# Kernel tuning notes

Measured on AMD Instinct MI355X. Metric: run time of the kernel, lower is better.

Reference implementation:

```python
import jax, jax.numpy as jnp
import numpy as np

H = 1024       # hiddenDim
MAXLEN = 512   # maxLen (encoder length)
VOCAB = 32000  # outDim (global in original source)


def setup_inputs() -> dict:
    key = jax.random.key(0)
    ks = jax.random.split(key, 12)
    s = 1.0 / np.sqrt(H)
    u = lambda k, shape: jax.random.uniform(k, shape, jnp.float32, -s, s)
    return {
        "inputId": jax.random.randint(ks[0], (1,), 0, VOCAB),
        "hidden": jax.random.normal(ks[1], (1, 1, H), jnp.float32),
        "encoderOuts": jax.random.normal(ks[2], (MAXLEN, H), jnp.float32),
        "embed_table": jax.random.normal(ks[3], (VOCAB, H), jnp.float32),
        "attn_w": u(ks[4], (MAXLEN, 2 * H)),
        "attn_b": u(ks[5], (MAXLEN,)),
        "comb_w": u(ks[6], (H, 2 * H)),
        "comb_b": u(ks[7], (H,)),
        "w_ih": u(ks[8], (3 * H, H)),
        "w_hh": u(ks[9], (3 * H, H)),
        "b_ih": u(ks[10], (3 * H,)),
        "b_hh": u(ks[11], (3 * H,)),
    }


def reference(inputId, hidden, encoderOuts, embed_table, attn_w, attn_b,
              comb_w, comb_b, w_ih, w_hh, b_ih, b_hh):
    # embedding + (eval-mode) dropout -> identity
    embed = embed_table[inputId].reshape(1, 1, -1)            # (1,1,H)
    # attention over encoder outputs
    cat = jnp.concatenate([embed[0], hidden[0]], axis=1)      # (1,2H)
    attnWeights = jax.nn.softmax(cat @ attn_w.T + attn_b, axis=1)  # (1,MAXLEN)
    attnApplied = attnWeights @ encoderOuts                   # (1,H) == bmm squeeze
    # combine + relu
    x = jnp.concatenate([embed[0], attnApplied], axis=1)      # (1,2H)
    x = jax.nn.relu(x @ comb_w.T + comb_b)                    # (1,H)
    # single GRU step; original calls self.rnn(out) with NO hidden -> h0 = zeros
    h0 = jnp.zeros_like(x)
    gi = x @ w_ih.T + b_ih                                    # (1,3H)
    gh = h0 @ w_hh.T + b_hh                                   # (1,3H)
    i_r, i_z, i_n = jnp.split(gi, 3, axis=1)
    h_r, h_z, h_n = jnp.split(gh, 3, axis=1)
    r = jax.nn.sigmoid(i_r + h_r)
    z = jax.nn.sigmoid(i_z + h_z)
    n = jnp.tanh(i_n + r * h_n)
    h_new = (1.0 - z) * n + z * h0                            # (1,H)
    out = jax.nn.sigmoid(h_new)[None]                         # (1,1,H)
    return out, h_new[None], attnWeights
```

## Files before the change

kernel.cpp:

```cpp
#include <hip/hip_runtime.h>
#include <hip/hip_bf16.h>

#define H 1024
#define MAXLEN 512

__device__ __forceinline__ float wave_reduce_sum(float a) {
    #pragma unroll
    for (int off = 32; off; off >>= 1) a += __shfl_xor(a, off);
    return a;
}
__device__ __forceinline__ float wave_reduce_max(float a) {
    #pragma unroll
    for (int off = 32; off; off >>= 1) a = fmaxf(a, __shfl_xor(a, off));
    return a;
}

__global__ void kA_logits(const int* __restrict__ inputId,
                          const float* __restrict__ embed_table,
                          const float* __restrict__ hidden,
                          const float* __restrict__ attn_w,
                          const float* __restrict__ attn_b,
                          float* __restrict__ logits) {
    int lane = threadIdx.x & 63;
    int row = blockIdx.x * 4 + (threadIdx.x >> 6);
    const float* embed = embed_table + (size_t)inputId[0] * H;
    const float* wrow = attn_w + (size_t)row * (2 * H);
    float acc = 0.f;
    #pragma unroll
    for (int it = 0; it < 8; ++it) {
        int base = it * 256 + lane * 4;
        float4 wv = *reinterpret_cast<const float4*>(wrow + base);
        float4 cv = (it < 4)
            ? *reinterpret_cast<const float4*>(embed + base)
            : *reinterpret_cast<const float4*>(hidden + (base - H));
        acc += wv.x * cv.x + wv.y * cv.y + wv.z * cv.z + wv.w * cv.w;
    }
    acc = wave_reduce_sum(acc);
    if (lane == 0) logits[row] = acc + attn_b[row];
}

__global__ void kB_softmax_apply(const float* __restrict__ logits,
                                 const float* __restrict__ enc,
                                 float* __restrict__ attnApplied,
                                 float* __restrict__ out_w) {
    __shared__ float w_lds[MAXLEN];
    __shared__ float red[4];
    __shared__ float part[8][32];
    int tid = threadIdx.x;
    int lane = tid & 63, wid = tid >> 6;

    float l0 = logits[tid];
    float l1 = logits[tid + 256];

    float m = wave_reduce_max(fmaxf(l0, l1));
    if (lane == 0) red[wid] = m;
    __syncthreads();
    m = fmaxf(fmaxf(red[0], red[1]), fmaxf(red[2], red[3]));
    __syncthreads();

    float e0 = expf(l0 - m), e1 = expf(l1 - m);

    float s = wave_reduce_sum(e0 + e1);
    if (lane == 0) red[wid] = s;
    __syncthreads();
    s = red[0] + red[1] + red[2] + red[3];
    float inv = 1.f / s;

    float w0 = e0 * inv, w1 = e1 * inv;
    w_lds[tid] = w0;
    w_lds[tid + 256] = w1;
    if (blockIdx.x == 0) {
        out_w[tid] = w0;
        out_w[tid + 256] = w1;
    }
    __syncthreads();

    int c = tid & 31;
    int ks = tid >> 5;
    int col = blockIdx.x * 32 + c;
    float acc = 0.f;
    for (int k = ks; k < MAXLEN; k += 8)
        acc += w_lds[k] * enc[(size_t)k * H + col];
    part[ks][c] = acc;
    __syncthreads();
    if (tid < 32) {
        float t = 0.f;
        #pragma unroll
        for (int i = 0; i < 8; ++i) t += part[i][tid];
        attnApplied[blockIdx.x * 32 + tid] = t;
    }
}

__global__ void kC_combine(const int* __restrict__ inputId,
                           const float* __restrict__ embed_table,
                           const float* __restrict__ attnApplied,
                           const float* __restrict__ comb_w,
                           const float* __restrict__ comb_b,
                           float* __restrict__ x) {
    int lane = threadIdx.x & 63;
    int row = blockIdx.x * 4 + (threadIdx.x >> 6);
    const float* embed = embed_table + (size_t)inputId[0] * H;
    const float* wrow = comb_w + (size_t)row * (2 * H);
    float acc = 0.f;
    #pragma unroll
    for (int it = 0; it < 8; ++it) {
        int base = it * 256 + lane * 4;
        float4 wv = *reinterpret_cast<const float4*>(wrow + base);
        float4 cv = (it < 4)
            ? *reinterpret_cast<const float4*>(embed + base)
            : *reinterpret_cast<const float4*>(attnApplied + (base - H));
        acc += wv.x * cv.x + wv.y * cv.y + wv.z * cv.z + wv.w * cv.w;
    }
    acc = wave_reduce_sum(acc);
    if (lane == 0) x[row] = fmaxf(acc + comb_b[row], 0.f);
}

__global__ void kD_gru(const float* __restrict__ w_ih,
                       const float* __restrict__ b_ih,
                       const float* __restrict__ b_hh,
                       const float* __restrict__ x,
                       float* __restrict__ d_out) {
    int lane = threadIdx.x & 63;
    int j = blockIdx.x * 4 + (threadIdx.x >> 6);
    float acc0 = 0.f, acc1 = 0.f, acc2 = 0.f;
    const float* wr = w_ih + (size_t)j * H;
    const float* wz = w_ih + (size_t)(H + j) * H;
    const float* wn = w_ih + (size_t)(2 * H + j) * H;
    #pragma unroll
    for (int it = 0; it < 4; ++it) {
        int base = it * 256 + lane * 4;
        float4 xv = *reinterpret_cast<const float4*>(x + base);
        float4 a = *reinterpret_cast<const float4*>(wr + base);
        float4 b = *reinterpret_cast<const float4*>(wz + base);
        float4 c = *reinterpret_cast<const float4*>(wn + base);
        acc0 += a.x * xv.x + a.y * xv.y + a.z * xv.z + a.w * xv.w;
        acc1 += b.x * xv.x + b.y * xv.y + b.z * xv.z + b.w * xv.w;
        acc2 += c.x * xv.x + c.y * xv.y + c.z * xv.z + c.w * xv.w;
    }
    #pragma unroll
    for (int off = 32; off; off >>= 1) {
        acc0 += __shfl_xor(acc0, off);
        acc1 += __shfl_xor(acc1, off);
        acc2 += __shfl_xor(acc2, off);
    }
    if (lane == 0) {
        float gi_r = acc0 + b_ih[j];
        float gi_z = acc1 + b_ih[H + j];
        float gi_n = acc2 + b_ih[2 * H + j];
        float r = 1.f / (1.f + expf(-(gi_r + b_hh[j])));
        float z = 1.f / (1.f + expf(-(gi_z + b_hh[H + j])));
        float n = tanhf(gi_n + r * b_hh[2 * H + j]);
        float hnew = (1.f - z) * n;
        float outv = 1.f / (1.f + expf(-hnew));
        d_out[j] = outv;
        d_out[H + j] = hnew;
    }
}

extern "C" void kernel_launch(void* const* d_in, const int* in_sizes, int n_in,
                              void* d_out, int out_size, void* d_ws, size_t ws_size,
                              hipStream_t stream) {
    const int*   inputId     = (const int*)d_in[0];
    const float* hidden      = (const float*)d_in[1];
    const float* enc         = (const float*)d_in[2];
    const float* embed_table = (const float*)d_in[3];
    const float* attn_w      = (const float*)d_in[4];
    const float* attn_b      = (const float*)d_in[5];
    const float* comb_w      = (const float*)d_in[6];
    const float* comb_b      = (const float*)d_in[7];
    const float* w_ih        = (const float*)d_in[8];
    const float* b_ih        = (const float*)d_in[10];
    const float* b_hh        = (const float*)d_in[11];

    float* out = (float*)d_out;
    float* ws  = (float*)d_ws;

    float* logits      = ws;
    float* attnApplied = ws + 512;
    float* x           = ws + 2048;

    kA_logits       <<<128, 256, 0, stream>>>(inputId, embed_table, hidden, attn_w, attn_b, logits);
    kB_softmax_apply<<<32,  256, 0, stream>>>(logits, enc, attnApplied, out + 2048);
    kC_combine      <<<256, 256, 0, stream>>>(inputId, embed_table, attnApplied, comb_w, comb_b, x);
    kD_gru          <<<256, 256, 0, stream>>>(w_ih, b_ih, b_hh, x, out);
}
```

Before: 24.32 us.

## Precompute comb_w×encoderOuts product with bf16 MFMA to remove serial attention stage

Reassociates comb_w[:,H:] @ (attnWeights @ enc) as (comb_w[:,H:] @ enc^T) @ attnWeights. A 1024x512x1024 bf16 MFMA GEMM computes that product in parallel with the attention logits and the embedding half of the combine matvec, so the launches drop from four to three. This removes the serial attention-apply and combine stages, but does about 1 GFLOP of extra matrix work per call, writes and reads a 2 MB intermediate, and lowers precision to bf16. The new path runs only if the workspace is large enough; otherwise the original four kernels run.

```diff
diff --git a/kernel.cpp b/kernel.cpp
--- a/kernel.cpp
+++ b/kernel.cpp
@@ -4,6 +4,10 @@
 #define H 1024
 #define MAXLEN 512
 
+typedef __bf16 bf16x8 __attribute__((ext_vector_type(8)));
+typedef __bf16 bf16x4 __attribute__((ext_vector_type(4)));
+typedef float  f32x4  __attribute__((ext_vector_type(4)));
+
 __device__ __forceinline__ float wave_reduce_sum(float a) {
     #pragma unroll
     for (int off = 32; off; off >>= 1) a += __shfl_xor(a, off);
@@ -15,111 +19,182 @@
     return a;
 }
 
-__global__ void kA_logits(const int* __restrict__ inputId,
-                          const float* __restrict__ embed_table,
-                          const float* __restrict__ hidden,
-                          const float* __restrict__ attn_w,
-                          const float* __restrict__ attn_b,
-                          float* __restrict__ logits) {
-    int lane = threadIdx.x & 63;
-    int row = blockIdx.x * 4 + (threadIdx.x >> 6);
+#define WS_LOGITS 0
+#define WS_Y1     512
+#define WS_Z      1536
+#define WS_GT     2560
+#define WS_FLOATS (2560 + 1024 * 512)
+
+__global__ __launch_bounds__(512)
+void node1(const int* __restrict__ inputId,
+           const float* __restrict__ hidden,
+           const float* __restrict__ enc,
+           const float* __restrict__ embed_table,
+           const float* __restrict__ attn_w,
+           const float* __restrict__ attn_b,
+           const float* __restrict__ comb_w,
+           const float* __restrict__ comb_b,
+           float* __restrict__ ws) {
+    float* logits = ws + WS_LOGITS;
+    float* y1     = ws + WS_Y1;
+    float* Gt     = ws + WS_GT;
+
+    __shared__ __bf16 lds_a[128][64];
+    __shared__ __bf16 lds_b[128][64];
+
+    const int tid  = threadIdx.x;
+    const int lane = tid & 63;
+    const int w    = tid >> 6;
+    const int b    = blockIdx.x;
+
     const float* embed = embed_table + (size_t)inputId[0] * H;
-    const float* wrow = attn_w + (size_t)row * (2 * H);
-    float acc = 0.f;
-    #pragma unroll
-    for (int it = 0; it < 8; ++it) {
-        int base = it * 256 + lane * 4;
-        float4 wv = *reinterpret_cast<const float4*>(wrow + base);
-        float4 cv = (it < 4)
-            ? *reinterpret_cast<const float4*>(embed + base)
-            : *reinterpret_cast<const float4*>(hidden + (base - H));
-        acc += wv.x * cv.x + wv.y * cv.y + wv.z * cv.z + wv.w * cv.w;
-    }
-    acc = wave_reduce_sum(acc);
-    if (lane == 0) logits[row] = acc + attn_b[row];
-}
-
-__global__ void kB_softmax_apply(const float* __restrict__ logits,
-                                 const float* __restrict__ enc,
-                                 float* __restrict__ attnApplied,
-                                 float* __restrict__ out_w) {
-    __shared__ float w_lds[MAXLEN];
+
+    if (b < 32) {
+        const int pBase = (b >> 2) * 128;
+        const int qBase = (b & 3) * 128;
+        const int wm = w & 3;
+        const int wn = w >> 2;
+        f32x4 acc[2][4];
+        #pragma unroll
+        for (int m = 0; m < 2; ++m)
+            #pragma unroll
+            for (int n = 0; n < 4; ++n) acc[m][n] = (f32x4){0.f, 0.f, 0.f, 0.f};
+
+        for (int c = 0; c < 16; ++c) {
+            const int k0 = c * 64;
+            #pragma unroll
+            for (int i = 0; i < 4; ++i) {
+                int f4  = tid + i * 512;
+                int row = f4 >> 4, c4 = f4 & 15;
+                float4 ga = *(const float4*)(comb_w + (size_t)(pBase + row) * 2048 + 1024 + k0 + c4 * 4);
+                float4 gb = *(const float4*)(enc    + (size_t)(qBase + row) * 1024 +        k0 + c4 * 4);
+                int off = ((((c4 >> 1) ^ (row & 7)) << 4) | ((c4 & 1) << 3));
+                bf16x4 va, vb;
+                va[0] = (__bf16)ga.x; va[1] = (__bf16)ga.y; va[2] = (__bf16)ga.z; va[3] = (__bf16)ga.w;
+                vb[0] = (__bf16)gb.x; vb[1] = (__bf16)gb.y; vb[2] = (__bf16)gb.z; vb[3] = (__bf16)gb.w;
+                *(bf16x4*)((char*)(&lds_a[row][0]) + off) = va;
+                *(bf16x4*)((char*)(&lds_b[row][0]) + off) = vb;
+            }
+            __syncthreads();
+            #pragma unroll
+            for (int ks = 0; ks < 2; ++ks) {
+                const int slot = ks * 4 + (lane >> 4);
+                bf16x8 af[2], bfr[4];
+                #pragma unroll
+                for (int m = 0; m < 2; ++m) {
+                    int row = wm * 32 + m * 16 + (lane & 15);
+                    af[m] = *(const bf16x8*)((const char*)(&lds_a[row][0]) + ((slot ^ (row & 7)) << 4));
+                }
+                #pragma unroll
+                for (int n = 0; n < 4; ++n) {
+                    int row = wn * 64 + n * 16 + (lane & 15);
+                    bfr[n] = *(const bf16x8*)((const char*)(&lds_b[row][0]) + ((slot ^ (row & 7)) << 4));
+                }
+                #pragma unroll
+                for (int m = 0; m < 2; ++m)
+                    #pragma unroll
+                    for (int n = 0; n < 4; ++n)
+                        acc[m][n] = __builtin_amdgcn_mfma_f32_16x16x32_bf16(af[m], bfr[n], acc[m][n], 0, 0, 0);
+            }
+            __syncthreads();
+        }
+        #pragma unroll
+        for (int m = 0; m < 2; ++m) {
+            int p0 = pBase + wm * 32 + m * 16 + (lane >> 4) * 4;
+            #pragma unroll
+            for (int n = 0; n < 4; ++n) {
+                int q = qBase + wn * 64 + n * 16 + (lane & 15);
+                #pragma unroll
+                for (int i = 0; i < 4; ++i)
+                    Gt[(size_t)(p0 + i) * 512 + q] = acc[m][n][i];
+            }
+        }
+    } else if (b < 96) {
+        int row = (b - 32) * 8 + w;
+        const float* wrow = attn_w + (size_t)row * (2 * H);
+        float acc = 0.f;
+        #pragma unroll
+        for (int it = 0; it < 8; ++it) {
+            int base = it * 256 + lane * 4;
+            float4 wv = *(const float4*)(wrow + base);
+            float4 cv = (it < 4) ? *(const float4*)(embed + base)
+                                 : *(const float4*)(hidden + (base - H));
+            acc += wv.x * cv.x + wv.y * cv.y + wv.z * cv.z + wv.w * cv.w;
+        }
+        acc = wave_reduce_sum(acc);
+        if (lane == 0) logits[row] = acc + attn_b[row];
+    } else {
+        #pragma unroll
+        for (int rr = 0; rr < 2; ++rr) {
+            int row = (b - 96) * 16 + w * 2 + rr;
+            const float* wrow = comb_w + (size_t)row * (2 * H);
+            float acc = 0.f;
+            #pragma unroll
+            for (int it = 0; it < 4; ++it) {
+                int base = it * 256 + lane * 4;
+                float4 wv = *(const float4*)(wrow + base);
+                float4 ev = *(const float4*)(embed + base);
+                acc += wv.x * ev.x + wv.y * ev.y + wv.z * ev.z + wv.w * ev.w;
+            }
+            acc = wave_reduce_sum(acc);
+            if (lane == 0) y1[row] = acc + comb_b[row];
+        }
+    }
+}
+
+__global__ __launch_bounds__(256)
+void node2(float* __restrict__ ws, float* __restrict__ d_out) {
+    const float* logits = ws + WS_LOGITS;
+    const float* y1     = ws + WS_Y1;
+    const float* Gt     = ws + WS_GT;
+    float* z = ws + WS_Z;
+
+    __shared__ float wsm[MAXLEN];
     __shared__ float red[4];
-    __shared__ float part[8][32];
-    int tid = threadIdx.x;
-    int lane = tid & 63, wid = tid >> 6;
-
-    float l0 = logits[tid];
-    float l1 = logits[tid + 256];
-
+    const int tid = threadIdx.x, lane = tid & 63, wid = tid >> 6;
+    const int b = blockIdx.x;
+
+    float l0 = logits[tid], l1 = logits[tid + 256];
     float m = wave_reduce_max(fmaxf(l0, l1));
     if (lane == 0) red[wid] = m;
     __syncthreads();
     m = fmaxf(fmaxf(red[0], red[1]), fmaxf(red[2], red[3]));
     __syncthreads();
-
     float e0 = expf(l0 - m), e1 = expf(l1 - m);
-
     float s = wave_reduce_sum(e0 + e1);
     if (lane == 0) red[wid] = s;
     __syncthreads();
     s = red[0] + red[1] + red[2] + red[3];
     float inv = 1.f / s;
-
     float w0 = e0 * inv, w1 = e1 * inv;
-    w_lds[tid] = w0;
-    w_lds[tid + 256] = w1;
-    if (blockIdx.x == 0) {
-        out_w[tid] = w0;
-        out_w[tid + 256] = w1;
-    }
-    __syncthreads();
-
-    int c = tid & 31;
-    int ks = tid >> 5;
-    int col = blockIdx.x * 32 + c;
-    float acc = 0.f;
-    for (int k = ks; k < MAXLEN; k += 8)
-        acc += w_lds[k] * enc[(size_t)k * H + col];
-    part[ks][c] = acc;
-    __syncthreads();
-    if (tid < 32) {
-        float t = 0.f;
-        #pragma unroll
-        for (int i = 0; i < 8; ++i) t += part[i][tid];
-        attnApplied[blockIdx.x * 32 + tid] = t;
-    }
-}
-
-__global__ void kC_combine(const int* __restrict__ inputId,
-                           const float* __restrict__ embed_table,
-                           const float* __restrict__ attnApplied,
-                           const float* __restrict__ comb_w,
-                           const float* __restrict__ comb_b,
-                           float* __restrict__ x) {
-    int lane = threadIdx.x & 63;
-    int row = blockIdx.x * 4 + (threadIdx.x >> 6);
-    const float* embed = embed_table + (size_t)inputId[0] * H;
-    const float* wrow = comb_w + (size_t)row * (2 * H);
-    float acc = 0.f;
-    #pragma unroll
-    for (int it = 0; it < 8; ++it) {
-        int base = it * 256 + lane * 4;
-        float4 wv = *reinterpret_cast<const float4*>(wrow + base);
-        float4 cv = (it < 4)
-            ? *reinterpret_cast<const float4*>(embed + base)
-            : *reinterpret_cast<const float4*>(attnApplied + (base - H));
-        acc += wv.x * cv.x + wv.y * cv.y + wv.z * cv.z + wv.w * cv.w;
-    }
-    acc = wave_reduce_sum(acc);
-    if (lane == 0) x[row] = fmaxf(acc + comb_b[row], 0.f);
-}
-
-__global__ void kD_gru(const float* __restrict__ w_ih,
-                       const float* __restrict__ b_ih,
-                       const float* __restrict__ b_hh,
-                       const float* __restrict__ x,
-                       float* __restrict__ d_out) {
+    wsm[tid] = w0;
+    wsm[tid + 256] = w1;
+    if (b == 0) {
+        d_out[2048 + tid] = w0;
+        d_out[2048 + 256 + tid] = w1;
+    }
+    __syncthreads();
+
+    #pragma unroll
+    for (int rr = 0; rr < 4; ++rr) {
+        int row = b * 16 + wid * 4 + rr;
+        const float* g = Gt + (size_t)row * 512;
+        float acc = 0.f;
+        #pragma unroll
+        for (int i = 0; i < 8; ++i)
+            acc += g[lane + 64 * i] * wsm[lane + 64 * i];
+        acc = wave_reduce_sum(acc);
+        if (lane == 0) z[row] = y1[row] + acc;
+    }
+}
+
+__global__ __launch_bounds__(256)
+void node3(const float* __restrict__ w_ih,
+           const float* __restrict__ b_ih,
+           const float* __restrict__ b_hh,
+           const float* __restrict__ ws,
+           float* __restrict__ d_out) {
+    const float* z = ws + WS_Z;
     int lane = threadIdx.x & 63;
     int j = blockIdx.x * 4 + (threadIdx.x >> 6);
     float acc0 = 0.f, acc1 = 0.f, acc2 = 0.f;
@@ -129,13 +204,128 @@
     #pragma unroll
     for (int it = 0; it < 4; ++it) {
         int base = it * 256 + lane * 4;
-        float4 xv = *reinterpret_cast<const float4*>(x + base);
-        float4 a = *reinterpret_cast<const float4*>(wr + base);
-        float4 b = *reinterpret_cast<const float4*>(wz + base);
-        float4 c = *reinterpret_cast<const float4*>(wn + base);
+        float4 xv = *(const float4*)(z + base);
+        xv.x = fmaxf(xv.x, 0.f); xv.y = fmaxf(xv.y, 0.f);
+        xv.z = fmaxf(xv.z, 0.f); xv.w = fmaxf(xv.w, 0.f);
+        float4 a = *(const float4*)(wr + base);
+        float4 c = *(const float4*)(wz + base);
+        float4 d = *(const float4*)(wn + base);
         acc0 += a.x * xv.x + a.y * xv.y + a.z * xv.z + a.w * xv.w;
-        acc1 += b.x * xv.x + b.y * xv.y + b.z * xv.z + b.w * xv.w;
-        acc2 += c.x * xv.x + c.y * xv.y + c.z * xv.z + c.w * xv.w;
+        acc1 += c.x * xv.x + c.y * xv.y + c.z * xv.z + c.w * xv.w;
+        acc2 += d.x * xv.x + d.y * xv.y + d.z * xv.z + d.w * xv.w;
+    }
+    #pragma unroll
+    for (int off = 32; off; off >>= 1) {
+        acc0 += __shfl_xor(acc0, off);
+        acc1 += __shfl_xor(acc1, off);
+        acc2 += __shfl_xor(acc2, off);
+    }
+    if (lane == 0) {
+        float gi_r = acc0 + b_ih[j];
+        float gi_z = acc1 + b_ih[H + j];
+        float gi_n = acc2 + b_ih[2 * H + j];
+        float r = 1.f / (1.f + expf(-(gi_r + b_hh[j])));
+        float zz = 1.f / (1.f + expf(-(gi_z + b_hh[H + j])));
+        float n = tanhf(gi_n + r * b_hh[2 * H + j]);
+        float hnew = (1.f - zz) * n;
+        float outv = 1.f / (1.f + expf(-hnew));
+        d_out[j] = outv;
+        d_out[H + j] = hnew;
+    }
+}
+
+__global__ void fb_kA(const int* __restrict__ inputId, const float* __restrict__ embed_table,
+                      const float* __restrict__ hidden, const float* __restrict__ attn_w,
+                      const float* __restrict__ attn_b, float* __restrict__ logits) {
+    int lane = threadIdx.x & 63;
+    int row = blockIdx.x * 4 + (threadIdx.x >> 6);
+    const float* embed = embed_table + (size_t)inputId[0] * H;
+    const float* wrow = attn_w + (size_t)row * (2 * H);
+    float acc = 0.f;
+    #pragma unroll
+    for (int it = 0; it < 8; ++it) {
+        int base = it * 256 + lane * 4;
+        float4 wv = *(const float4*)(wrow + base);
+        float4 cv = (it < 4) ? *(const float4*)(embed + base)
+                             : *(const float4*)(hidden + (base - H));
+        acc += wv.x * cv.x + wv.y * cv.y + wv.z * cv.z + wv.w * cv.w;
+    }
+    acc = wave_reduce_sum(acc);
+    if (lane == 0) logits[row] = acc + attn_b[row];
+}
+__global__ void fb_kB(const float* __restrict__ logits, const float* __restrict__ enc,
+                      float* __restrict__ attnApplied, float* __restrict__ out_w) {
+    __shared__ float w_lds[MAXLEN];
+    __shared__ float red[4];
+    __shared__ float part[8][32];
+    int tid = threadIdx.x, lane = tid & 63, wid = tid >> 6;
+    float l0 = logits[tid], l1 = logits[tid + 256];
+    float m = wave_reduce_max(fmaxf(l0, l1));
+    if (lane == 0) red[wid] = m;
+    __syncthreads();
+    m = fmaxf(fmaxf(red[0], red[1]), fmaxf(red[2], red[3]));
+    __syncthreads();
+    float e0 = expf(l0 - m), e1 = expf(l1 - m);
+    float s = wave_reduce_sum(e0 + e1);
+    if (lane == 0) red[wid] = s;
+    __syncthreads();
+    s = red[0] + red[1] + red[2] + red[3];
+    float inv = 1.f / s;
+    float w0 = e0 * inv, w1 = e1 * inv;
+    w_lds[tid] = w0; w_lds[tid + 256] = w1;
+    if (blockIdx.x == 0) { out_w[tid] = w0; out_w[tid + 256] = w1; }
+    __syncthreads();
+    int c = tid & 31, ks = tid >> 5;
+    int col = blockIdx.x * 32 + c;
+    float acc = 0.f;
+    for (int k = ks; k < MAXLEN; k += 8) acc += w_lds[k] * enc[(size_t)k * H + col];
+    part[ks][c] = acc;
+    __syncthreads();
+    if (tid < 32) {
+        float t = 0.f;
+        #pragma unroll
+        for (int i = 0; i < 8; ++i) t += part[i][tid];
+        attnApplied[blockIdx.x * 32 + tid] = t;
+    }
+}
+__global__ void fb_kC(const int* __restrict__ inputId, const float* __restrict__ embed_table,
+                      const float* __restrict__ attnApplied, const float* __restrict__ comb_w,
+                      const float* __restrict__ comb_b, float* __restrict__ x) {
+    int lane = threadIdx.x & 63;
+    int row = blockIdx.x * 4 + (threadIdx.x >> 6);
+    const float* embed = embed_table + (size_t)inputId[0] * H;
+    const float* wrow = comb_w + (size_t)row * (2 * H);
+    float acc = 0.f;
+    #pragma unroll
+    for (int it = 0; it < 8; ++it) {
+        int base = it * 256 + lane * 4;
+        float4 wv = *(const float4*)(wrow + base);
+        float4 cv = (it < 4) ? *(const float4*)(embed + base)
+                             : *(const float4*)(attnApplied + (base - H));
+        acc += wv.x * cv.x + wv.y * cv.y + wv.z * cv.z + wv.w * cv.w;
+    }
+    acc = wave_reduce_sum(acc);
+    if (lane == 0) x[row] = fmaxf(acc + comb_b[row], 0.f);
+}
+__global__ void fb_kD(const float* __restrict__ w_ih, const float* __restrict__ b_ih,
+                      const float* __restrict__ b_hh, const float* __restrict__ x,
+                      float* __restrict__ d_out) {
+    int lane = threadIdx.x & 63;
+    int j = blockIdx.x * 4 + (threadIdx.x >> 6);
+    float acc0 = 0.f, acc1 = 0.f, acc2 = 0.f;
+    const float* wr = w_ih + (size_t)j * H;
+    const float* wz = w_ih + (size_t)(H + j) * H;
+    const float* wn = w_ih + (size_t)(2 * H + j) * H;
+    #pragma unroll
+    for (int it = 0; it < 4; ++it) {
+        int base = it * 256 + lane * 4;
+        float4 xv = *(const float4*)(x + base);
+        float4 a = *(const float4*)(wr + base);
+        float4 c = *(const float4*)(wz + base);
+        float4 d = *(const float4*)(wn + base);
+        acc0 += a.x * xv.x + a.y * xv.y + a.z * xv.z + a.w * xv.w;
+        acc1 += c.x * xv.x + c.y * xv.y + c.z * xv.z + c.w * xv.w;
+        acc2 += d.x * xv.x + d.y * xv.y + d.z * xv.z + d.w * xv.w;
     }
     #pragma unroll
     for (int off = 32; off; off >>= 1) {
@@ -175,12 +365,18 @@
     float* out = (float*)d_out;
     float* ws  = (float*)d_ws;
 
-    float* logits      = ws;
-    float* attnApplied = ws + 512;
-    float* x           = ws + 2048;
-
-    kA_logits       <<<128, 256, 0, stream>>>(inputId, embed_table, hidden, attn_w, attn_b, logits);
-    kB_softmax_apply<<<32,  256, 0, stream>>>(logits, enc, attnApplied, out + 2048);
-    kC_combine      <<<256, 256, 0, stream>>>(inputId, embed_table, attnApplied, comb_w, comb_b, x);
-    kD_gru          <<<256, 256, 0, stream>>>(w_ih, b_ih, b_hh, x, out);
-}
+    if (ws_size >= (size_t)WS_FLOATS * sizeof(float)) {
+        node1<<<160, 512, 0, stream>>>(inputId, hidden, enc, embed_table,
+                                       attn_w, attn_b, comb_w, comb_b, ws);
+        node2<<<64, 256, 0, stream>>>(ws, out);
+        node3<<<256, 256, 0, stream>>>(w_ih, b_ih, b_hh, ws, out);
+    } else {
+        float* logits      = ws;
+        float* attnApplied = ws + 512;
+        float* x           = ws + 2048;
+        fb_kA<<<128, 256, 0, stream>>>(inputId, embed_table, hidden, attn_w, attn_b, logits);
+        fb_kB<<<32,  256, 0, stream>>>(logits, enc, attnApplied, out + 2048);
+        fb_kC<<<256, 256, 0, stream>>>(inputId, embed_table, attnApplied, comb_w, comb_b, x);
+        fb_kD<<<256, 256, 0, stream>>>(w_ih, b_ih, b_hh, x, out);
+    }
+}
```

Result: slower. 37.90 us (+55.8%).
